# Optimization experiments

Measured on AMD Instinct MI355X. Metric: run time of the kernel, lower is better.

Reference implementation:

```python
import jax, jax.numpy as jnp
import numpy as np

B, L, N, C = 64, 12, 4096, 3
FD, HD, OUT = 32, 64, 12
TID, DIW, TD = 288, 7, 16
STEPS = 4
EMB = 10  # node embedding dim for learned adjacency


def setup_inputs() -> dict:
    key = jax.random.key(0)
    ks = jax.random.split(key, 16)
    g = lambda i, shape, s=0.05: jax.random.normal(ks[i], shape, dtype=jnp.float32) * s
    z = lambda n: jnp.zeros((n,), jnp.float32)
    return {
        "history_data": jax.random.uniform(ks[0], (B, L, N, C), dtype=jnp.float32),
        "future_data": jnp.zeros((B, L, N, 1), jnp.float32),
        "batch_seen": 0,
        "epoch": 0,
        "train": 1,
        "tid_emb": g(1, (TID, TD)),
        "diw_emb": g(2, (DIW, TD)),
        "t2f_w": g(3, (2 * TD, FD)), "t2f_b": z(FD),
        "enc_w1": g(4, (L * C, HD)), "enc_b1": z(HD),
        "enc_w2": g(5, (HD, FD)), "enc_b2": z(FD),
        "node_emb": g(6, (N, EMB), 1.0),
        "pde_w1": g(7, (FD, HD)), "pde_b1": z(HD),
        "pde_w2": g(8, (HD, FD)), "pde_b2": z(FD),
        "ss_win": g(9, (FD, FD)), "ss_wst": g(10, (FD, FD)), "ss_b": z(FD),
        "ss_wout": g(11, (FD, FD)), "ss_bout": z(FD),
        "dec_w1": g(12, (FD, HD)), "dec_b1": z(HD),
        "dec_w2": g(13, (HD, OUT)), "dec_b2": z(OUT),
        "pde_mix": jnp.array(0.5, jnp.float32),
    }


def reference(history_data, future_data, batch_seen, epoch, train,
              tid_emb, diw_emb, t2f_w, t2f_b,
              enc_w1, enc_b1, enc_w2, enc_b2,
              node_emb,
              pde_w1, pde_b1, pde_w2, pde_b2,
              ss_win, ss_wst, ss_b, ss_wout, ss_bout,
              dec_w1, dec_b1, dec_w2, dec_b2, pde_mix):
    # --- encoder: per-node MLP over flattened (L, C) history ---
    x = history_data[..., :C]                                    # [B,L,N,C]
    x = jnp.transpose(x, (0, 2, 1, 3)).reshape(B, N, L * C)      # [B,N,L*C]
    field = jnp.maximum(x @ enc_w1 + enc_b1, 0.0) @ enc_w2 + enc_b2  # [B,N,FD]

    # --- temporal field bias from last-step tid/diw ---
    tid_idx = jnp.clip((history_data[:, -1, :, 1] * TID).astype(jnp.int32), 0, TID - 1)
    diw_idx = jnp.clip((history_data[:, -1, :, 2] * DIW).astype(jnp.int32), 0, DIW - 1)
    temp = jnp.concatenate([tid_emb[tid_idx], diw_emb[diw_idx]], axis=-1)  # [B,N,2*TD]
    field = field + temp @ t2f_w + t2f_b

    # --- learned adjacency for graph Laplacian (L = I - A) ---
    A = jax.nn.softmax(jnp.maximum(node_emb @ node_emb.T, 0.0), axis=-1)  # [N,N]

    alpha = jax.nn.sigmoid(pde_mix)
    dt = 1.0 / STEPS
    state = jnp.zeros_like(field)
    for _ in range(STEPS):  # fixed small unroll over PDE steps
        L_F = jnp.einsum('nm,bmf->bnf', A, field) - field         # (A - I) F
        N_F = jnp.maximum(field @ pde_w1 + pde_b1, 0.0) @ pde_w2 + pde_b2
        fe = field + (alpha * L_F + (1.0 - alpha) * N_F) * dt
        state = jnp.tanh(fe @ ss_win + state @ ss_wst + ss_b)     # state-space update
        field = fe + state @ ss_wout + ss_bout

    # --- decoder: per-node MLP to output horizon ---
    pred = jnp.maximum(field @ dec_w1 + dec_b1, 0.0) @ dec_w2 + dec_b2  # [B,N,OUT]
    return jnp.transpose(pred, (0, 2, 1))[..., None]              # [B,OUT,N,1]
```

## Files before the change

### kernel.cpp

```cpp
#include <hip/hip_runtime.h>

#define BATCH 64
#define LHIST 12
#define NNODE 4096
#define CCH   3
#define FD    32
#define HD    64
#define OUTD  12
#define TIDN  288
#define DIWN  7
#define TDD   16
#define EMBD  10
#define MROWS 2048
#define KDIM  4096
#define MTOT  (BATCH * NNODE)

typedef __attribute__((ext_vector_type(8))) short bf16x8;
typedef __attribute__((ext_vector_type(4))) float f32x4;

union BF8U { bf16x8 v; unsigned short s[8]; };

__device__ __forceinline__ unsigned short f2b(float f) {
    union { float f; unsigned u; } v; v.f = f;
    unsigned r = v.u + 0x7fffu + ((v.u >> 16) & 1u);
    return (unsigned short)(r >> 16);
}

__device__ __forceinline__ float b2f(unsigned short u) {
    union { unsigned u; float f; } v; v.u = (unsigned)u << 16; return v.f;
}

__device__ __forceinline__ float fast_tanh(float x) {
    x = fminf(fmaxf(x, -15.f), 15.f);
    const float e = __expf(2.f * x);
    return (e - 1.f) / (e + 1.f);
}

__device__ __forceinline__ bf16x8 ldsfrag(const unsigned short* p) {
    return *(const bf16x8*)p;
}

__device__ __forceinline__ bf16x8 pack8(float4 a, float4 b) {
    BF8U u;
    u.s[0] = f2b(a.x); u.s[1] = f2b(a.y); u.s[2] = f2b(a.z); u.s[3] = f2b(a.w);
    u.s[4] = f2b(b.x); u.s[5] = f2b(b.y); u.s[6] = f2b(b.z); u.s[7] = f2b(b.w);
    return u.v;
}

__global__ __launch_bounds__(256) void build_A(const float* __restrict__ emb,
                                               unsigned short* __restrict__ A) {
    const int n = blockIdx.x;
    const int tid = threadIdx.x;
    __shared__ float sc[NNODE];
    __shared__ float red[256];
    float e[EMBD];
#pragma unroll
    for (int c = 0; c < EMBD; c++) e[c] = emb[(size_t)n * EMBD + c];
    float mx = 0.f;
    for (int m = tid; m < NNODE; m += 256) {
        float s = 0.f;
#pragma unroll
        for (int c = 0; c < EMBD; c++) s += e[c] * emb[(size_t)m * EMBD + c];
        s = fmaxf(s, 0.f);
        sc[m] = s;
        mx = fmaxf(mx, s);
    }
    red[tid] = mx;
    __syncthreads();
    for (int off = 128; off > 0; off >>= 1) {
        if (tid < off) red[tid] = fmaxf(red[tid], red[tid + off]);
        __syncthreads();
    }
    mx = red[0];
    __syncthreads();
    float sum = 0.f;
    for (int m = tid; m < NNODE; m += 256) {
        float v = expf(sc[m] - mx);
        sc[m] = v;
        sum += v;
    }
    red[tid] = sum;
    __syncthreads();
    for (int off = 128; off > 0; off >>= 1) {
        if (tid < off) red[tid] += red[tid + off];
        __syncthreads();
    }
    const float inv = 1.f / red[0];
    for (int m = tid; m < NNODE; m += 256)
        A[(size_t)n * NNODE + m] = f2b(sc[m] * inv);
}

__global__ __launch_bounds__(256, 2) void encoder(const float* __restrict__ hist,
                                                  const float* __restrict__ tid_emb,
                                                  const float* __restrict__ diw_emb,
                                                  const float* __restrict__ t2f_w,
                                                  const float* __restrict__ t2f_b,
                                                  const float* __restrict__ enc_w1,
                                                  const float* __restrict__ enc_b1,
                                                  const float* __restrict__ enc_w2,
                                                  const float* __restrict__ enc_b2,
                                                  float* __restrict__ field,
                                                  unsigned short* __restrict__ fT) {
    const int gid = blockIdx.x * 256 + threadIdx.x;
    const int b = gid >> 12;
    const int n = gid & (NNODE - 1);
    const float* hb = hist + ((size_t)b * LHIST * NNODE + n) * CCH;
    float x[LHIST * CCH];
#pragma unroll
    for (int l = 0; l < LHIST; l++) {
        x[l * 3 + 0] = hb[(size_t)l * NNODE * CCH + 0];
        x[l * 3 + 1] = hb[(size_t)l * NNODE * CCH + 1];
        x[l * 3 + 2] = hb[(size_t)l * NNODE * CCH + 2];
    }
    float f[FD];
#pragma unroll
    for (int o = 0; o < FD; o++) f[o] = enc_b2[o] + t2f_b[o];
    for (int j = 0; j < HD; j++) {
        float h = enc_b1[j];
#pragma unroll
        for (int k = 0; k < LHIST * CCH; k++) h += x[k] * enc_w1[k * HD + j];
        h = fmaxf(h, 0.f);
#pragma unroll
        for (int o = 0; o < FD; o++) f[o] += h * enc_w2[j * FD + o];
    }
    const int ti = min(max((int)(x[11 * 3 + 1] * 288.0f), 0), TIDN - 1);
    const int di = min(max((int)(x[11 * 3 + 2] * 7.0f), 0), DIWN - 1);
    for (int g = 0; g < TDD; g++) {
        const float tg = tid_emb[ti * TDD + g];
        const float dg = diw_emb[di * TDD + g];
#pragma unroll
        for (int o = 0; o < FD; o++)
            f[o] += tg * t2f_w[g * FD + o] + dg * t2f_w[(TDD + g) * FD + o];
    }
#pragma unroll
    for (int o4 = 0; o4 < FD / 4; o4++) {
        float4 v = {f[o4 * 4 + 0], f[o4 * 4 + 1], f[o4 * 4 + 2], f[o4 * 4 + 3]};
        *(float4*)&field[(size_t)gid * FD + o4 * 4] = v;
    }
#pragma unroll
    for (int o = 0; o < FD; o++)
        fT[(size_t)(b * FD + o) * NNODE + n] = f2b(f[o]);
}

__global__ __launch_bounds__(256) void gemm_bt(const unsigned short* __restrict__ X,
                                               const unsigned short* __restrict__ Y,
                                               unsigned short* __restrict__ Cp) {
    constexpr int K = KDIM;
    constexpr int KS = KDIM / 2;
    constexpr int BK = 32;
    __shared__ __align__(16) unsigned short Xs[2][128 * BK];
    __shared__ __align__(16) unsigned short Ys[2][128 * BK];
    const int tid = threadIdx.x;
    const int wave = tid >> 6;
    const int lane = tid & 63;

    const int l = blockIdx.x + 16 * blockIdx.y;
    const int xcd = l & 7;
    const int rem = l >> 3;
    const int by = xcd * 4 + (rem & 3);
    const int bx = rem >> 2;
    const int i0 = bx * 128;
    const int j0 = by * 128;
    const int k0 = blockIdx.z * KS;
    unsigned short* C = Cp + (size_t)blockIdx.z * MTOT * FD;

    const int wi = (wave >> 1) * 64;
    const int wj = (wave & 1) * 64;

    const int lrow = lane >> 2;
    const int gcol = (lane & 3) * 8;
    const int scol = ((lane & 3) ^ ((lane >> 3) & 3)) * 8;

    const unsigned short* Xg = X + (size_t)(i0 + wave * 32 + lrow) * K + k0 + gcol;
    const unsigned short* Yg = Y + (size_t)(j0 + wave * 32 + lrow) * K + k0 + gcol;
    const int ldoff0 = (wave * 32 + lrow) * BK + scol;
    const int ldoff1 = (wave * 32 + 16 + lrow) * BK + scol;

    const f32x4 zero = {0.f, 0.f, 0.f, 0.f};
    f32x4 acc[4][4];
#pragma unroll
    for (int a = 0; a < 4; a++)
#pragma unroll
        for (int b = 0; b < 4; b++) acc[a][b] = zero;

    const int fr = lane & 15;
    const int q = lane >> 4;
    const int kq = (q ^ ((fr >> 1) & 3)) * 8;

    uint4 rx0 = *(const uint4*)(Xg);
    uint4 rx1 = *(const uint4*)(Xg + 16 * K);
    uint4 ry0 = *(const uint4*)(Yg);
    uint4 ry1 = *(const uint4*)(Yg + 16 * K);
    *(uint4*)&Xs[0][ldoff0] = rx0;
    *(uint4*)&Xs[0][ldoff1] = rx1;
    *(uint4*)&Ys[0][ldoff0] = ry0;
    *(uint4*)&Ys[0][ldoff1] = ry1;
    __syncthreads();

    int p = 0;
    for (int kt = 0; kt < KS; kt += BK) {
        const bool more = (kt + BK < KS);
        if (more) {
            rx0 = *(const uint4*)(Xg + kt + BK);
            rx1 = *(const uint4*)(Xg + kt + BK + 16 * K);
            ry0 = *(const uint4*)(Yg + kt + BK);
            ry1 = *(const uint4*)(Yg + kt + BK + 16 * K);
        }
        bf16x8 fa[4], fb[4];
#pragma unroll
        for (int t = 0; t < 4; t++)
            fa[t] = *(const bf16x8*)&Xs[p][(wi + t * 16 + fr) * BK + kq];
#pragma unroll
        for (int t = 0; t < 4; t++)
            fb[t] = *(const bf16x8*)&Ys[p][(wj + t * 16 + fr) * BK + kq];
#pragma unroll
        for (int mi = 0; mi < 4; mi++)
#pragma unroll
            for (int ni = 0; ni < 4; ni++)
                acc[mi][ni] = __builtin_amdgcn_mfma_f32_16x16x32_bf16(
                    fa[mi], fb[ni], acc[mi][ni], 0, 0, 0);
        if (more) {
            const int np = p ^ 1;
            *(uint4*)&Xs[np][ldoff0] = rx0;
            *(uint4*)&Xs[np][ldoff1] = rx1;
            *(uint4*)&Ys[np][ldoff0] = ry0;
            *(uint4*)&Ys[np][ldoff1] = ry1;
            __syncthreads();
            p = np;
        }
    }

    const int r0 = q * 4;
#pragma unroll
    for (int mi = 0; mi < 4; mi++) {
#pragma unroll
        for (int ni = 0; ni < 4; ni++) {
            const int R0 = i0 + wi + mi * 16 + r0;
            const int col = j0 + wj + ni * 16 + fr;
            const size_t addr = ((size_t)(R0 >> 5) * NNODE + col) * FD + (R0 & 31);
            ushort4 pk = {f2b(acc[mi][ni][0]), f2b(acc[mi][ni][1]),
                          f2b(acc[mi][ni][2]), f2b(acc[mi][ni][3])};
            *(ushort4*)&C[addr] = pk;
        }
    }
}

#define HPAD 72
#define FPAD 40
__global__ __launch_bounds__(256, 2) void step_mfma(const unsigned short* __restrict__ Ct0,
                                                    const unsigned short* __restrict__ Ct1,
                                                    float* __restrict__ field,
                                                    unsigned short* __restrict__ state,
                                                    unsigned short* __restrict__ fT,
                                                    const float* __restrict__ pde_w1,
                                                    const float* __restrict__ pde_b1,
                                                    const float* __restrict__ pde_w2,
                                                    const float* __restrict__ pde_b2,
                                                    const float* __restrict__ ss_win,
                                                    const float* __restrict__ ss_wst,
                                                    const float* __restrict__ ss_b,
                                                    const float* __restrict__ ss_wout,
                                                    const float* __restrict__ ss_bout,
                                                    const float* __restrict__ pde_mix,
                                                    const float* __restrict__ dec_w1,
                                                    const float* __restrict__ dec_b1,
                                                    const float* __restrict__ dec_w2,
                                                    const float* __restrict__ dec_b2,
                                                    float* __restrict__ out,
                                                    int first, int last) {
    __shared__ __align__(16) unsigned short W1T[HD * FD];
    __shared__ __align__(16) unsigned short W2T[FD * HD];
    __shared__ __align__(16) unsigned short WinT[FD * FD];
    __shared__ __align__(16) unsigned short WstT[FD * FD];
    __shared__ __align__(16) unsigned short WoutT[FD * FD];
    __shared__ __align__(16) unsigned short Wd1T[HD * FD];
    __shared__ __align__(16) unsigned short Wd2T[16 * HD];
    __shared__ __align__(16) unsigned short Hs[4 * 64 * HPAD];
    __shared__ __align__(16) unsigned short Fs[4 * 64 * FPAD];

    const int tid = threadIdx.x;
    for (int i = tid; i < HD * FD; i += 256) W1T[(i & 63) * FD + (i >> 6)] = f2b(pde_w1[i]);
    for (int i = tid; i < HD * FD; i += 256) W2T[(i & 31) * HD + (i >> 5)] = f2b(pde_w2[i]);
    for (int i = tid; i < FD * FD; i += 256) {
        WinT [(i & 31) * FD + (i >> 5)] = f2b(ss_win[i]);
        WstT [(i & 31) * FD + (i >> 5)] = f2b(ss_wst[i]);
        WoutT[(i & 31) * FD + (i >> 5)] = f2b(ss_wout[i]);
    }
    if (last) {
        for (int i = tid; i < HD * FD; i += 256)
            Wd1T[(i & 63) * FD + (i >> 6)] = f2b(dec_w1[i]);
        for (int i = tid; i < 16 * HD; i += 256) {
            const int o = i >> 6, j = i & 63;
            Wd2T[i] = (o < OUTD) ? f2b(dec_w2[j * OUTD + o]) : (unsigned short)0;
        }
    }
    __syncthreads();

    const int wv = tid >> 6;
    const int lane = tid & 63;
    const int ln = lane & 15;
    const int q = lane >> 4;
    const int kq = q * 8;
    const int r0 = q * 4;
    const int mw = blockIdx.x * 256 + wv * 64;
    const int b = mw >> 12;
    const int n0 = mw & (NNODE - 1);
    unsigned short* Hw = &Hs[wv * 64 * HPAD];
    unsigned short* Fw = &Fs[wv * 64 * FPAD];

    const float alpha = 1.f / (1.f + __expf(-pde_mix[0]));
    const float dt = 0.25f;

    bf16x8 w1f[4], w2f[2][2], winf[2], wstf[2], woutf[2];
#pragma unroll
    for (int nj = 0; nj < 4; nj++) w1f[nj] = ldsfrag(&W1T[(nj * 16 + ln) * FD + kq]);
#pragma unroll
    for (int nf = 0; nf < 2; nf++) {
#pragma unroll
        for (int kk = 0; kk < 2; kk++)
            w2f[nf][kk] = ldsfrag(&W2T[(nf * 16 + ln) * HD + kk * 32 + kq]);
        winf[nf]  = ldsfrag(&WinT [(nf * 16 + ln) * FD + kq]);
        wstf[nf]  = ldsfrag(&WstT [(nf * 16 + ln) * FD + kq]);
        woutf[nf] = ldsfrag(&WoutT[(nf * 16 + ln) * FD + kq]);
    }

    float b1v[4], b2v[2], bsv[2], bov[2];
#pragma unroll
    for (int nj = 0; nj < 4; nj++) b1v[nj] = pde_b1[nj * 16 + ln];
#pragma unroll
    for (int nf = 0; nf < 2; nf++) {
        b2v[nf] = pde_b2[nf * 16 + ln];
        bsv[nf] = ss_b[nf * 16 + ln];
        bov[nf] = ss_bout[nf * 16 + ln];
    }

    bf16x8 fA[4], stA[4];
#pragma unroll
    for (int mi = 0; mi < 4; mi++) {
        const float4* fp = (const float4*)&field[(size_t)(mw + mi * 16 + ln) * FD + kq];
        fA[mi] = pack8(fp[0], fp[1]);
    }
    if (!first) {
#pragma unroll
        for (int mi = 0; mi < 4; mi++)
            stA[mi] = *(const bf16x8*)&state[(size_t)(mw + mi * 16 + ln) * FD + kq];
    }

    const f32x4 zero = {0.f, 0.f, 0.f, 0.f};

    f32x4 hc[4][4];
#pragma unroll
    for (int mi = 0; mi < 4; mi++)
#pragma unroll
        for (int nj = 0; nj < 4; nj++)
            hc[mi][nj] = __builtin_amdgcn_mfma_f32_16x16x32_bf16(fA[mi], w1f[nj], zero, 0, 0, 0);
#pragma unroll
    for (int mi = 0; mi < 4; mi++)
#pragma unroll
        for (int nj = 0; nj < 4; nj++)
#pragma unroll
            for (int r = 0; r < 4; r++)
                Hw[(mi * 16 + r0 + r) * HPAD + nj * 16 + ln] =
                    f2b(fmaxf(hc[mi][nj][r] + b1v[nj], 0.f));

    float fld[4][2][4], ctv[4][2][4];
#pragma unroll
    for (int mi = 0; mi < 4; mi++)
#pragma unroll
        for (int nf = 0; nf < 2; nf++)
#pragma unroll
            for (int r = 0; r < 4; r++) {
                const size_t idx = (size_t)(mw + mi * 16 + r0 + r) * FD + nf * 16 + ln;
                fld[mi][nf][r] = field[idx];
                ctv[mi][nf][r] = b2f(Ct0[idx]) + b2f(Ct1[idx]);
            }

    bf16x8 hA[4][2];
#pragma unroll
    for (int mi = 0; mi < 4; mi++)
#pragma unroll
        for (int kk = 0; kk < 2; kk++)
            hA[mi][kk] = ldsfrag(&Hw[(mi * 16 + ln) * HPAD + kk * 32 + kq]);
    f32x4 nc[4][2];
#pragma unroll
    for (int mi = 0; mi < 4; mi++)
#pragma unroll
        for (int nf = 0; nf < 2; nf++) {
            f32x4 a = __builtin_amdgcn_mfma_f32_16x16x32_bf16(hA[mi][0], w2f[nf][0], zero, 0, 0, 0);
            nc[mi][nf] = __builtin_amdgcn_mfma_f32_16x16x32_bf16(hA[mi][1], w2f[nf][1], a, 0, 0, 0);
        }

    float fe[4][2][4];
#pragma unroll
    for (int mi = 0; mi < 4; mi++)
#pragma unroll
        for (int nf = 0; nf < 2; nf++)
#pragma unroll
            for (int r = 0; r < 4; r++) {
                const float nfv = nc[mi][nf][r] + b2v[nf];
                const float fv = fld[mi][nf][r];
                fe[mi][nf][r] = fv + (alpha * (ctv[mi][nf][r] - fv) + (1.f - alpha) * nfv) * dt;
                Fw[(mi * 16 + r0 + r) * FPAD + nf * 16 + ln] = f2b(fe[mi][nf][r]);
            }

    bf16x8 feA[4];
#pragma unroll
    for (int mi = 0; mi < 4; mi++) feA[mi] = ldsfrag(&Fw[(mi * 16 + ln) * FPAD + kq]);
    f32x4 sc_[4][2];
#pragma unroll
    for (int mi = 0; mi < 4; mi++)
#pragma unroll
        for (int nf = 0; nf < 2; nf++) {
            f32x4 a = __builtin_amdgcn_mfma_f32_16x16x32_bf16(feA[mi], winf[nf], zero, 0, 0, 0);
            if (!first)
                a = __builtin_amdgcn_mfma_f32_16x16x32_bf16(stA[mi], wstf[nf], a, 0, 0, 0);
            sc_[mi][nf] = a;
        }
    float sval[4][2][4];
#pragma unroll
    for (int mi = 0; mi < 4; mi++)
#pragma unroll
        for (int nf = 0; nf < 2; nf++)
#pragma unroll
            for (int r = 0; r < 4; r++)
                sval[mi][nf][r] = fast_tanh(sc_[mi][nf][r] + bsv[nf]);
#pragma unroll
    for (int mi = 0; mi < 4; mi++)
#pragma unroll
        for (int nf = 0; nf < 2; nf++)
#pragma unroll
            for (int r = 0; r < 4; r++)
                Fw[(mi * 16 + r0 + r) * FPAD + nf * 16 + ln] = f2b(sval[mi][nf][r]);

    bf16x8 SA[4];
#pragma unroll
    for (int mi = 0; mi < 4; mi++) SA[mi] = ldsfrag(&Fw[(mi * 16 + ln) * FPAD + kq]);
    float fnew[4][2][4];
#pragma unroll
    for (int mi = 0; mi < 4; mi++)
#pragma unroll
        for (int nf = 0; nf < 2; nf++) {
            f32x4 oc = __builtin_amdgcn_mfma_f32_16x16x32_bf16(SA[mi], woutf[nf], zero, 0, 0, 0);
#pragma unroll
            for (int r = 0; r < 4; r++)
                fnew[mi][nf][r] = fe[mi][nf][r] + oc[r] + bov[nf];
        }

    if (!last) {
#pragma unroll
        for (int mi = 0; mi < 4; mi++) {
#pragma unroll
            for (int nf = 0; nf < 2; nf++) {
#pragma unroll
                for (int r = 0; r < 4; r++) {
                    const size_t idx = (size_t)(mw + mi * 16 + r0 + r) * FD + nf * 16 + ln;
                    field[idx] = fnew[mi][nf][r];
                    state[idx] = f2b(sval[mi][nf][r]);
                }
                ushort4 pk = {f2b(fnew[mi][nf][0]), f2b(fnew[mi][nf][1]),
                              f2b(fnew[mi][nf][2]), f2b(fnew[mi][nf][3])};
                const size_t ft_addr = (size_t)(b * FD + nf * 16 + ln) * NNODE + n0 + mi * 16 + r0;
                *(ushort4*)&fT[ft_addr] = pk;
            }
        }
    } else {
        bf16x8 wd1f[4], wd2f[2];
#pragma unroll
        for (int nj = 0; nj < 4; nj++) wd1f[nj] = ldsfrag(&Wd1T[(nj * 16 + ln) * FD + kq]);
#pragma unroll
        for (int kk = 0; kk < 2; kk++) wd2f[kk] = ldsfrag(&Wd2T[ln * HD + kk * 32 + kq]);
        float db1v[4];
#pragma unroll
        for (int nj = 0; nj < 4; nj++) db1v[nj] = dec_b1[nj * 16 + ln];
        const float db2v = (ln < OUTD) ? dec_b2[ln] : 0.f;

#pragma unroll
        for (int mi = 0; mi < 4; mi++)
#pragma unroll
            for (int nf = 0; nf < 2; nf++)
#pragma unroll
                for (int r = 0; r < 4; r++)
                    Fw[(mi * 16 + r0 + r) * FPAD + nf * 16 + ln] = f2b(fnew[mi][nf][r]);
        bf16x8 fnA[4];
#pragma unroll
        for (int mi = 0; mi < 4; mi++) fnA[mi] = ldsfrag(&Fw[(mi * 16 + ln) * FPAD + kq]);

        f32x4 h2[4][4];
#pragma unroll
        for (int mi = 0; mi < 4; mi++)
#pragma unroll
            for (int nj = 0; nj < 4; nj++)
                h2[mi][nj] = __builtin_amdgcn_mfma_f32_16x16x32_bf16(fnA[mi], wd1f[nj], zero, 0, 0, 0);
#pragma unroll
        for (int mi = 0; mi < 4; mi++)
#pragma unroll
            for (int nj = 0; nj < 4; nj++)
#pragma unroll
                for (int r = 0; r < 4; r++)
                    Hw[(mi * 16 + r0 + r) * HPAD + nj * 16 + ln] =
                        f2b(fmaxf(h2[mi][nj][r] + db1v[nj], 0.f));
        bf16x8 h2A[4][2];
#pragma unroll
        for (int mi = 0; mi < 4; mi++)
#pragma unroll
            for (int kk = 0; kk < 2; kk++)
                h2A[mi][kk] = ldsfrag(&Hw[(mi * 16 + ln) * HPAD + kk * 32 + kq]);
#pragma unroll
        for (int mi = 0; mi < 4; mi++) {
            f32x4 a = __builtin_amdgcn_mfma_f32_16x16x32_bf16(h2A[mi][0], wd2f[0], zero, 0, 0, 0);
            a = __builtin_amdgcn_mfma_f32_16x16x32_bf16(h2A[mi][1], wd2f[1], a, 0, 0, 0);
            if (ln < OUTD) {
                float4 v = {a[0] + db2v, a[1] + db2v, a[2] + db2v, a[3] + db2v};
                *(float4*)&out[(size_t)(b * OUTD + ln) * NNODE + n0 + mi * 16 + r0] = v;
            }
        }
    }
}

extern "C" void kernel_launch(void* const* d_in, const int* in_sizes, int n_in,
                              void* d_out, int out_size, void* d_ws, size_t ws_size,
                              hipStream_t stream) {
    (void)in_sizes; (void)n_in; (void)out_size; (void)ws_size;
    const float* hist    = (const float*)d_in[0];
    const float* tid_emb = (const float*)d_in[5];
    const float* diw_emb = (const float*)d_in[6];
    const float* t2f_w   = (const float*)d_in[7];
    const float* t2f_b   = (const float*)d_in[8];
    const float* enc_w1  = (const float*)d_in[9];
    const float* enc_b1  = (const float*)d_in[10];
    const float* enc_w2  = (const float*)d_in[11];
    const float* enc_b2  = (const float*)d_in[12];
    const float* node_emb= (const float*)d_in[13];
    const float* pde_w1  = (const float*)d_in[14];
    const float* pde_b1  = (const float*)d_in[15];
    const float* pde_w2  = (const float*)d_in[16];
    const float* pde_b2  = (const float*)d_in[17];
    const float* ss_win  = (const float*)d_in[18];
    const float* ss_wst  = (const float*)d_in[19];
    const float* ss_b    = (const float*)d_in[20];
    const float* ss_wout = (const float*)d_in[21];
    const float* ss_bout = (const float*)d_in[22];
    const float* dec_w1  = (const float*)d_in[23];
    const float* dec_b1  = (const float*)d_in[24];
    const float* dec_w2  = (const float*)d_in[25];
    const float* dec_b2  = (const float*)d_in[26];
    const float* pde_mix = (const float*)d_in[27];

    char* w = (char*)d_ws;
    unsigned short* A_bf = (unsigned short*)w;  w += (size_t)KDIM * KDIM * 2;
    unsigned short* fT   = (unsigned short*)w;  w += (size_t)MROWS * KDIM * 2;
    float* field = (float*)w;                   w += (size_t)MTOT * FD * 4;
    unsigned short* state = (unsigned short*)w; w += (size_t)MTOT * FD * 2;
    unsigned short* Cp    = (unsigned short*)w; w += (size_t)2 * MTOT * FD * 2;

    build_A<<<NNODE, 256, 0, stream>>>(node_emb, A_bf);
    encoder<<<(BATCH * NNODE) / 256, 256, 0, stream>>>(hist, tid_emb, diw_emb, t2f_w,
                                                       t2f_b, enc_w1, enc_b1, enc_w2,
                                                       enc_b2, field, fT);
    for (int s = 0; s < 4; s++) {
        gemm_bt<<<dim3(16, 32, 2), 256, 0, stream>>>(fT, A_bf, Cp);
        step_mfma<<<MTOT / 256, 256, 0, stream>>>(
            Cp, Cp + (size_t)MTOT * FD, field, state, fT, pde_w1, pde_b1, pde_w2,
            pde_b2, ss_win, ss_wst, ss_b, ss_wout, ss_bout, pde_mix,
            dec_w1, dec_b1, dec_w2, dec_b2, (float*)d_out,
            s == 0 ? 1 : 0, s == 3 ? 1 : 0);
    }
}
```

Baseline: 732.0 us.

## Fuse adjacency GEMM with PDE step epilogue and merge init kernels

Fuses the A·F GEMM and the per-node PDE/state-space step into one kernel. Each GEMM tile runs its own epilogue from LDS-transposed accumulators, which removes the split-K partial buffer and its round-trip through global memory. Tile loads now go through global_load_lds direct-to-LDS copies, and the fT buffer is ping-ponged so the next step's input can be written while other blocks still read the old one. The adjacency build and the encoder are merged into one launch. In exchange, split-K is dropped, leaving 512 blocks each running the full K loop, and LDS use per block goes up.

```diff
diff --git a/kernel.cpp b/kernel.cpp
--- a/kernel.cpp
+++ b/kernel.cpp
@@ -36,6 +36,11 @@
     return (e - 1.f) / (e + 1.f);
 }
 
+__device__ __forceinline__ void gl2lds16(const void* g, void* l) {
+    __builtin_amdgcn_global_load_lds((__attribute__((address_space(1))) void*)(void*)g,
+                                     (__attribute__((address_space(3))) void*)l, 16, 0, 0);
+}
+
 __device__ __forceinline__ bf16x8 ldsfrag(const unsigned short* p) {
     return *(const bf16x8*)p;
 }
@@ -47,112 +52,156 @@
     return u.v;
 }
 
-__global__ __launch_bounds__(256) void build_A(const float* __restrict__ emb,
-                                               unsigned short* __restrict__ A) {
-    const int n = blockIdx.x;
-    const int tid = threadIdx.x;
+__global__ __launch_bounds__(256, 2) void init_k(const float* __restrict__ emb,
+                                                 unsigned short* __restrict__ A,
+                                                 const float* __restrict__ hist,
+                                                 const float* __restrict__ tid_emb,
+                                                 const float* __restrict__ diw_emb,
+                                                 const float* __restrict__ t2f_w,
+                                                 const float* __restrict__ t2f_b,
+                                                 const float* __restrict__ enc_w1,
+                                                 const float* __restrict__ enc_b1,
+                                                 const float* __restrict__ enc_w2,
+                                                 const float* __restrict__ enc_b2,
+                                                 float* __restrict__ field,
+                                                 unsigned short* __restrict__ fT) {
     __shared__ float sc[NNODE];
     __shared__ float red[256];
-    float e[EMBD];
-#pragma unroll
-    for (int c = 0; c < EMBD; c++) e[c] = emb[(size_t)n * EMBD + c];
-    float mx = 0.f;
-    for (int m = tid; m < NNODE; m += 256) {
-        float s = 0.f;
-#pragma unroll
-        for (int c = 0; c < EMBD; c++) s += e[c] * emb[(size_t)m * EMBD + c];
-        s = fmaxf(s, 0.f);
-        sc[m] = s;
-        mx = fmaxf(mx, s);
-    }
-    red[tid] = mx;
-    __syncthreads();
-    for (int off = 128; off > 0; off >>= 1) {
-        if (tid < off) red[tid] = fmaxf(red[tid], red[tid + off]);
+    const int tid = threadIdx.x;
+    if (blockIdx.x < NNODE) {
+        const int n = blockIdx.x;
+        float e[EMBD];
+#pragma unroll
+        for (int c = 0; c < EMBD; c++) e[c] = emb[(size_t)n * EMBD + c];
+        float mx = 0.f;
+        for (int m = tid; m < NNODE; m += 256) {
+            float s = 0.f;
+#pragma unroll
+            for (int c = 0; c < EMBD; c++) s += e[c] * emb[(size_t)m * EMBD + c];
+            s = fmaxf(s, 0.f);
+            sc[m] = s;
+            mx = fmaxf(mx, s);
+        }
+        red[tid] = mx;
         __syncthreads();
-    }
-    mx = red[0];
-    __syncthreads();
-    float sum = 0.f;
-    for (int m = tid; m < NNODE; m += 256) {
-        float v = expf(sc[m] - mx);
-        sc[m] = v;
-        sum += v;
-    }
-    red[tid] = sum;
-    __syncthreads();
-    for (int off = 128; off > 0; off >>= 1) {
-        if (tid < off) red[tid] += red[tid + off];
+        for (int off = 128; off > 0; off >>= 1) {
+            if (tid < off) red[tid] = fmaxf(red[tid], red[tid + off]);
+            __syncthreads();
+        }
+        mx = red[0];
         __syncthreads();
-    }
-    const float inv = 1.f / red[0];
-    for (int m = tid; m < NNODE; m += 256)
-        A[(size_t)n * NNODE + m] = f2b(sc[m] * inv);
-}
-
-__global__ __launch_bounds__(256, 2) void encoder(const float* __restrict__ hist,
-                                                  const float* __restrict__ tid_emb,
-                                                  const float* __restrict__ diw_emb,
-                                                  const float* __restrict__ t2f_w,
-                                                  const float* __restrict__ t2f_b,
-                                                  const float* __restrict__ enc_w1,
-                                                  const float* __restrict__ enc_b1,
-                                                  const float* __restrict__ enc_w2,
-                                                  const float* __restrict__ enc_b2,
-                                                  float* __restrict__ field,
-                                                  unsigned short* __restrict__ fT) {
-    const int gid = blockIdx.x * 256 + threadIdx.x;
-    const int b = gid >> 12;
-    const int n = gid & (NNODE - 1);
-    const float* hb = hist + ((size_t)b * LHIST * NNODE + n) * CCH;
-    float x[LHIST * CCH];
-#pragma unroll
-    for (int l = 0; l < LHIST; l++) {
-        x[l * 3 + 0] = hb[(size_t)l * NNODE * CCH + 0];
-        x[l * 3 + 1] = hb[(size_t)l * NNODE * CCH + 1];
-        x[l * 3 + 2] = hb[(size_t)l * NNODE * CCH + 2];
-    }
-    float f[FD];
-#pragma unroll
-    for (int o = 0; o < FD; o++) f[o] = enc_b2[o] + t2f_b[o];
-    for (int j = 0; j < HD; j++) {
-        float h = enc_b1[j];
-#pragma unroll
-        for (int k = 0; k < LHIST * CCH; k++) h += x[k] * enc_w1[k * HD + j];
-        h = fmaxf(h, 0.f);
-#pragma unroll
-        for (int o = 0; o < FD; o++) f[o] += h * enc_w2[j * FD + o];
-    }
-    const int ti = min(max((int)(x[11 * 3 + 1] * 288.0f), 0), TIDN - 1);
-    const int di = min(max((int)(x[11 * 3 + 2] * 7.0f), 0), DIWN - 1);
-    for (int g = 0; g < TDD; g++) {
-        const float tg = tid_emb[ti * TDD + g];
-        const float dg = diw_emb[di * TDD + g];
+        float sum = 0.f;
+        for (int m = tid; m < NNODE; m += 256) {
+            float v = expf(sc[m] - mx);
+            sc[m] = v;
+            sum += v;
+        }
+        red[tid] = sum;
+        __syncthreads();
+        for (int off = 128; off > 0; off >>= 1) {
+            if (tid < off) red[tid] += red[tid + off];
+            __syncthreads();
+        }
+        const float inv = 1.f / red[0];
+        for (int m = tid; m < NNODE; m += 256)
+            A[(size_t)n * NNODE + m] = f2b(sc[m] * inv);
+    } else {
+        const int gid = (blockIdx.x - NNODE) * 256 + tid;
+        const int b = gid >> 12;
+        const int n = gid & (NNODE - 1);
+        const float* hb = hist + ((size_t)b * LHIST * NNODE + n) * CCH;
+        float x[LHIST * CCH];
+#pragma unroll
+        for (int l = 0; l < LHIST; l++) {
+            x[l * 3 + 0] = hb[(size_t)l * NNODE * CCH + 0];
+            x[l * 3 + 1] = hb[(size_t)l * NNODE * CCH + 1];
+            x[l * 3 + 2] = hb[(size_t)l * NNODE * CCH + 2];
+        }
+        float f[FD];
+#pragma unroll
+        for (int o = 0; o < FD; o++) f[o] = enc_b2[o] + t2f_b[o];
+        for (int j = 0; j < HD; j++) {
+            float h = enc_b1[j];
+#pragma unroll
+            for (int k = 0; k < LHIST * CCH; k++) h += x[k] * enc_w1[k * HD + j];
+            h = fmaxf(h, 0.f);
+#pragma unroll
+            for (int o = 0; o < FD; o++) f[o] += h * enc_w2[j * FD + o];
+        }
+        const int ti = min(max((int)(x[11 * 3 + 1] * 288.0f), 0), TIDN - 1);
+        const int di = min(max((int)(x[11 * 3 + 2] * 7.0f), 0), DIWN - 1);
+        for (int g = 0; g < TDD; g++) {
+            const float tg = tid_emb[ti * TDD + g];
+            const float dg = diw_emb[di * TDD + g];
+#pragma unroll
+            for (int o = 0; o < FD; o++)
+                f[o] += tg * t2f_w[g * FD + o] + dg * t2f_w[(TDD + g) * FD + o];
+        }
+#pragma unroll
+        for (int o4 = 0; o4 < FD / 4; o4++) {
+            float4 v = {f[o4 * 4 + 0], f[o4 * 4 + 1], f[o4 * 4 + 2], f[o4 * 4 + 3]};
+            *(float4*)&field[(size_t)gid * FD + o4 * 4] = v;
+        }
 #pragma unroll
         for (int o = 0; o < FD; o++)
-            f[o] += tg * t2f_w[g * FD + o] + dg * t2f_w[(TDD + g) * FD + o];
-    }
-#pragma unroll
-    for (int o4 = 0; o4 < FD / 4; o4++) {
-        float4 v = {f[o4 * 4 + 0], f[o4 * 4 + 1], f[o4 * 4 + 2], f[o4 * 4 + 3]};
-        *(float4*)&field[(size_t)gid * FD + o4 * 4] = v;
-    }
-#pragma unroll
-    for (int o = 0; o < FD; o++)
-        fT[(size_t)(b * FD + o) * NNODE + n] = f2b(f[o]);
-}
-
-__global__ __launch_bounds__(256) void gemm_bt(const unsigned short* __restrict__ X,
-                                               const unsigned short* __restrict__ Y,
-                                               unsigned short* __restrict__ Cp) {
+            fT[(size_t)(b * FD + o) * NNODE + n] = f2b(f[o]);
+    }
+}
+
+#define TPAD 36
+#define QHP  72
+#define QFP  40
+__global__ __launch_bounds__(256) void gemm_step(const unsigned short* __restrict__ X,
+                                                 const unsigned short* __restrict__ Y,
+                                                 float* __restrict__ field,
+                                                 unsigned short* __restrict__ state,
+                                                 unsigned short* __restrict__ fTo,
+                                                 const float* __restrict__ pde_w1,
+                                                 const float* __restrict__ pde_b1,
+                                                 const float* __restrict__ pde_w2,
+                                                 const float* __restrict__ pde_b2,
+                                                 const float* __restrict__ ss_win,
+                                                 const float* __restrict__ ss_wst,
+                                                 const float* __restrict__ ss_b,
+                                                 const float* __restrict__ ss_wout,
+                                                 const float* __restrict__ ss_bout,
+                                                 const float* __restrict__ pde_mix,
+                                                 const float* __restrict__ dec_w1,
+                                                 const float* __restrict__ dec_b1,
+                                                 const float* __restrict__ dec_w2,
+                                                 const float* __restrict__ dec_b2,
+                                                 float* __restrict__ out,
+                                                 int first, int last) {
     constexpr int K = KDIM;
-    constexpr int KS = KDIM / 2;
     constexpr int BK = 32;
-    __shared__ __align__(16) unsigned short Xs[2][128 * BK];
-    __shared__ __align__(16) unsigned short Ys[2][128 * BK];
+    __shared__ __align__(16) unsigned short SM0[512 * TPAD];
+    __shared__ __align__(16) unsigned short W1T[HD * FD];
+    __shared__ __align__(16) unsigned short W2T[FD * HD];
+    __shared__ __align__(16) unsigned short WinT[FD * FD];
+    __shared__ __align__(16) unsigned short WstT[FD * FD];
+    __shared__ __align__(16) unsigned short WoutT[FD * FD];
+    __shared__ __align__(16) unsigned short Hs[4 * 32 * QHP];
+    __shared__ __align__(16) unsigned short Fs[4 * 32 * QFP];
+
     const int tid = threadIdx.x;
     const int wave = tid >> 6;
     const int lane = tid & 63;
+
+    for (int i = tid; i < HD * FD; i += 256) W1T[(i & 63) * FD + (i >> 6)] = f2b(pde_w1[i]);
+    for (int i = tid; i < HD * FD; i += 256) W2T[(i & 31) * HD + (i >> 5)] = f2b(pde_w2[i]);
+    for (int i = tid; i < FD * FD; i += 256) {
+        WinT [(i & 31) * FD + (i >> 5)] = f2b(ss_win[i]);
+        WstT [(i & 31) * FD + (i >> 5)] = f2b(ss_wst[i]);
+        WoutT[(i & 31) * FD + (i >> 5)] = f2b(ss_wout[i]);
+    }
+    if (last) {
+        for (int i = tid; i < HD * FD; i += 256)
+            Hs[(i & 63) * FD + (i >> 6)] = f2b(dec_w1[i]);
+        for (int i = tid; i < 16 * HD; i += 256) {
+            const int o = i >> 6, j = i & 63;
+            Hs[HD * FD + i] = (o < OUTD) ? f2b(dec_w2[j * OUTD + o]) : (unsigned short)0;
+        }
+    }
 
     const int l = blockIdx.x + 16 * blockIdx.y;
     const int xcd = l & 7;
@@ -161,20 +210,22 @@
     const int bx = rem >> 2;
     const int i0 = bx * 128;
     const int j0 = by * 128;
-    const int k0 = blockIdx.z * KS;
-    unsigned short* C = Cp + (size_t)blockIdx.z * MTOT * FD;
+    const int b0 = i0 >> 5;
 
     const int wi = (wave >> 1) * 64;
     const int wj = (wave & 1) * 64;
 
     const int lrow = lane >> 2;
-    const int gcol = (lane & 3) * 8;
-    const int scol = ((lane & 3) ^ ((lane >> 3) & 3)) * 8;
-
-    const unsigned short* Xg = X + (size_t)(i0 + wave * 32 + lrow) * K + k0 + gcol;
-    const unsigned short* Yg = Y + (size_t)(j0 + wave * 32 + lrow) * K + k0 + gcol;
-    const int ldoff0 = (wave * 32 + lrow) * BK + scol;
-    const int ldoff1 = (wave * 32 + 16 + lrow) * BK + scol;
+    const int gcol = ((lane & 3) ^ ((lane >> 3) & 3)) * 8;
+
+    const unsigned short* Xg = X + (size_t)(i0 + wave * 32 + lrow) * K + gcol;
+    const unsigned short* Yg = Y + (size_t)(j0 + wave * 32 + lrow) * K + gcol;
+    unsigned short* XsB = SM0;
+    unsigned short* YsB = SM0 + 8192;
+    unsigned short* Xd0 = XsB + (wave * 32) * BK;
+    unsigned short* Xd1 = XsB + (wave * 32 + 16) * BK;
+    unsigned short* Yd0 = YsB + (wave * 32) * BK;
+    unsigned short* Yd1 = YsB + (wave * 32 + 16) * BK;
 
     const f32x4 zero = {0.f, 0.f, 0.f, 0.f};
     f32x4 acc[4][4];
@@ -185,129 +236,58 @@
 
     const int fr = lane & 15;
     const int q = lane >> 4;
-    const int kq = (q ^ ((fr >> 1) & 3)) * 8;
-
-    uint4 rx0 = *(const uint4*)(Xg);
-    uint4 rx1 = *(const uint4*)(Xg + 16 * K);
-    uint4 ry0 = *(const uint4*)(Yg);
-    uint4 ry1 = *(const uint4*)(Yg + 16 * K);
-    *(uint4*)&Xs[0][ldoff0] = rx0;
-    *(uint4*)&Xs[0][ldoff1] = rx1;
-    *(uint4*)&Ys[0][ldoff0] = ry0;
-    *(uint4*)&Ys[0][ldoff1] = ry1;
+    const int kq8 = (q ^ ((fr >> 1) & 3)) * 8;
+
+#define GS_ISSUE(P, KT)                                        \
+    gl2lds16(Xg + (KT), Xd0 + (P) * 4096);                     \
+    gl2lds16(Xg + (KT) + 16 * K, Xd1 + (P) * 4096);            \
+    gl2lds16(Yg + (KT), Yd0 + (P) * 4096);                     \
+    gl2lds16(Yg + (KT) + 16 * K, Yd1 + (P) * 4096);
+
+#define GS_COMPUTE(P)                                                                 \
+    {                                                                                 \
+        bf16x8 fa[4], fb[4];                                                          \
+        _Pragma("unroll") for (int t = 0; t < 4; t++)                                 \
+            fa[t] = *(const bf16x8*)&XsB[(P) * 4096 + (wi + t * 16 + fr) * BK + kq8]; \
+        _Pragma("unroll") for (int t = 0; t < 4; t++)                                 \
+            fb[t] = *(const bf16x8*)&YsB[(P) * 4096 + (wj + t * 16 + fr) * BK + kq8]; \
+        _Pragma("unroll") for (int mi = 0; mi < 4; mi++)                              \
+            _Pragma("unroll") for (int ni = 0; ni < 4; ni++)                          \
+                acc[mi][ni] = __builtin_amdgcn_mfma_f32_16x16x32_bf16(                \
+                    fa[mi], fb[ni], acc[mi][ni], 0, 0, 0);                            \
+    }
+
+    GS_ISSUE(0, 0);
     __syncthreads();
-
     int p = 0;
-    for (int kt = 0; kt < KS; kt += BK) {
-        const bool more = (kt + BK < KS);
-        if (more) {
-            rx0 = *(const uint4*)(Xg + kt + BK);
-            rx1 = *(const uint4*)(Xg + kt + BK + 16 * K);
-            ry0 = *(const uint4*)(Yg + kt + BK);
-            ry1 = *(const uint4*)(Yg + kt + BK + 16 * K);
-        }
-        bf16x8 fa[4], fb[4];
-#pragma unroll
-        for (int t = 0; t < 4; t++)
-            fa[t] = *(const bf16x8*)&Xs[p][(wi + t * 16 + fr) * BK + kq];
-#pragma unroll
-        for (int t = 0; t < 4; t++)
-            fb[t] = *(const bf16x8*)&Ys[p][(wj + t * 16 + fr) * BK + kq];
-#pragma unroll
-        for (int mi = 0; mi < 4; mi++)
-#pragma unroll
-            for (int ni = 0; ni < 4; ni++)
-                acc[mi][ni] = __builtin_amdgcn_mfma_f32_16x16x32_bf16(
-                    fa[mi], fb[ni], acc[mi][ni], 0, 0, 0);
-        if (more) {
-            const int np = p ^ 1;
-            *(uint4*)&Xs[np][ldoff0] = rx0;
-            *(uint4*)&Xs[np][ldoff1] = rx1;
-            *(uint4*)&Ys[np][ldoff0] = ry0;
-            *(uint4*)&Ys[np][ldoff1] = ry1;
-            __syncthreads();
-            p = np;
-        }
-    }
-
+    for (int kt = 0; kt < K; kt += BK) {
+        if (kt + BK < K) { GS_ISSUE(p ^ 1, kt + BK); }
+        GS_COMPUTE(p);
+        __syncthreads();
+        p ^= 1;
+    }
+#undef GS_COMPUTE
+#undef GS_ISSUE
+
+    unsigned short* T = SM0;
     const int r0 = q * 4;
 #pragma unroll
     for (int mi = 0; mi < 4; mi++) {
 #pragma unroll
         for (int ni = 0; ni < 4; ni++) {
             const int R0 = i0 + wi + mi * 16 + r0;
-            const int col = j0 + wj + ni * 16 + fr;
-            const size_t addr = ((size_t)(R0 >> 5) * NNODE + col) * FD + (R0 & 31);
+            const int nl = wj + ni * 16 + fr;
             ushort4 pk = {f2b(acc[mi][ni][0]), f2b(acc[mi][ni][1]),
                           f2b(acc[mi][ni][2]), f2b(acc[mi][ni][3])};
-            *(ushort4*)&C[addr] = pk;
-        }
-    }
-}
-
-#define HPAD 72
-#define FPAD 40
-__global__ __launch_bounds__(256, 2) void step_mfma(const unsigned short* __restrict__ Ct0,
-                                                    const unsigned short* __restrict__ Ct1,
-                                                    float* __restrict__ field,
-                                                    unsigned short* __restrict__ state,
-                                                    unsigned short* __restrict__ fT,
-                                                    const float* __restrict__ pde_w1,
-                                                    const float* __restrict__ pde_b1,
-                                                    const float* __restrict__ pde_w2,
-                                                    const float* __restrict__ pde_b2,
-                                                    const float* __restrict__ ss_win,
-                                                    const float* __restrict__ ss_wst,
-                                                    const float* __restrict__ ss_b,
-                                                    const float* __restrict__ ss_wout,
-                                                    const float* __restrict__ ss_bout,
-                                                    const float* __restrict__ pde_mix,
-                                                    const float* __restrict__ dec_w1,
-                                                    const float* __restrict__ dec_b1,
-                                                    const float* __restrict__ dec_w2,
-                                                    const float* __restrict__ dec_b2,
-                                                    float* __restrict__ out,
-                                                    int first, int last) {
-    __shared__ __align__(16) unsigned short W1T[HD * FD];
-    __shared__ __align__(16) unsigned short W2T[FD * HD];
-    __shared__ __align__(16) unsigned short WinT[FD * FD];
-    __shared__ __align__(16) unsigned short WstT[FD * FD];
-    __shared__ __align__(16) unsigned short WoutT[FD * FD];
-    __shared__ __align__(16) unsigned short Wd1T[HD * FD];
-    __shared__ __align__(16) unsigned short Wd2T[16 * HD];
-    __shared__ __align__(16) unsigned short Hs[4 * 64 * HPAD];
-    __shared__ __align__(16) unsigned short Fs[4 * 64 * FPAD];
-
-    const int tid = threadIdx.x;
-    for (int i = tid; i < HD * FD; i += 256) W1T[(i & 63) * FD + (i >> 6)] = f2b(pde_w1[i]);
-    for (int i = tid; i < HD * FD; i += 256) W2T[(i & 31) * HD + (i >> 5)] = f2b(pde_w2[i]);
-    for (int i = tid; i < FD * FD; i += 256) {
-        WinT [(i & 31) * FD + (i >> 5)] = f2b(ss_win[i]);
-        WstT [(i & 31) * FD + (i >> 5)] = f2b(ss_wst[i]);
-        WoutT[(i & 31) * FD + (i >> 5)] = f2b(ss_wout[i]);
-    }
-    if (last) {
-        for (int i = tid; i < HD * FD; i += 256)
-            Wd1T[(i & 63) * FD + (i >> 6)] = f2b(dec_w1[i]);
-        for (int i = tid; i < 16 * HD; i += 256) {
-            const int o = i >> 6, j = i & 63;
-            Wd2T[i] = (o < OUTD) ? f2b(dec_w2[j * OUTD + o]) : (unsigned short)0;
+            *(ushort4*)&T[((((R0 >> 5) & 3) << 7) + nl) * TPAD + (R0 & 31)] = pk;
         }
     }
     __syncthreads();
 
-    const int wv = tid >> 6;
-    const int lane = tid & 63;
-    const int ln = lane & 15;
-    const int q = lane >> 4;
+    const int ln = fr;
     const int kq = q * 8;
-    const int r0 = q * 4;
-    const int mw = blockIdx.x * 256 + wv * 64;
-    const int b = mw >> 12;
-    const int n0 = mw & (NNODE - 1);
-    unsigned short* Hw = &Hs[wv * 64 * HPAD];
-    unsigned short* Fw = &Fs[wv * 64 * FPAD];
-
+    unsigned short* Hw = &Hs[wave * 32 * QHP];
+    unsigned short* Fw = &Fs[wave * 32 * QFP];
     const float alpha = 1.f / (1.f + __expf(-pde_mix[0]));
     const float dt = 0.25f;
 
@@ -323,7 +303,6 @@
         wstf[nf]  = ldsfrag(&WstT [(nf * 16 + ln) * FD + kq]);
         woutf[nf] = ldsfrag(&WoutT[(nf * 16 + ln) * FD + kq]);
     }
-
     float b1v[4], b2v[2], bsv[2], bov[2];
 #pragma unroll
     for (int nj = 0; nj < 4; nj++) b1v[nj] = pde_b1[nj * 16 + ln];
@@ -334,184 +313,194 @@
         bov[nf] = ss_bout[nf * 16 + ln];
     }
 
-    bf16x8 fA[4], stA[4];
-#pragma unroll
-    for (int mi = 0; mi < 4; mi++) {
-        const float4* fp = (const float4*)&field[(size_t)(mw + mi * 16 + ln) * FD + kq];
-        fA[mi] = pack8(fp[0], fp[1]);
-    }
-    if (!first) {
-#pragma unroll
-        for (int mi = 0; mi < 4; mi++)
-            stA[mi] = *(const bf16x8*)&state[(size_t)(mw + mi * 16 + ln) * FD + kq];
-    }
-
-    const f32x4 zero = {0.f, 0.f, 0.f, 0.f};
-
-    f32x4 hc[4][4];
-#pragma unroll
-    for (int mi = 0; mi < 4; mi++)
-#pragma unroll
-        for (int nj = 0; nj < 4; nj++)
-            hc[mi][nj] = __builtin_amdgcn_mfma_f32_16x16x32_bf16(fA[mi], w1f[nj], zero, 0, 0, 0);
-#pragma unroll
-    for (int mi = 0; mi < 4; mi++)
-#pragma unroll
-        for (int nj = 0; nj < 4; nj++)
-#pragma unroll
-            for (int r = 0; r < 4; r++)
-                Hw[(mi * 16 + r0 + r) * HPAD + nj * 16 + ln] =
-                    f2b(fmaxf(hc[mi][nj][r] + b1v[nj], 0.f));
-
-    float fld[4][2][4], ctv[4][2][4];
-#pragma unroll
-    for (int mi = 0; mi < 4; mi++)
-#pragma unroll
-        for (int nf = 0; nf < 2; nf++)
-#pragma unroll
-            for (int r = 0; r < 4; r++) {
-                const size_t idx = (size_t)(mw + mi * 16 + r0 + r) * FD + nf * 16 + ln;
-                fld[mi][nf][r] = field[idx];
-                ctv[mi][nf][r] = b2f(Ct0[idx]) + b2f(Ct1[idx]);
+    bf16x8 wd1f[4], wd2f[2];
+    float db1v[4];
+    float db2v = 0.f;
+    if (last) {
+#pragma unroll
+        for (int nj = 0; nj < 4; nj++) wd1f[nj] = ldsfrag(&Hs[(nj * 16 + ln) * FD + kq]);
+#pragma unroll
+        for (int kk = 0; kk < 2; kk++) wd2f[kk] = ldsfrag(&Hs[HD * FD + ln * HD + kk * 32 + kq]);
+#pragma unroll
+        for (int nj = 0; nj < 4; nj++) db1v[nj] = dec_b1[nj * 16 + ln];
+        db2v = (ln < OUTD) ? dec_b2[ln] : 0.f;
+        __syncthreads();
+    }
+
+    for (int qtr = 0; qtr < 4; qtr++) {
+        const int lb = wave * 128 + qtr * 32;
+        const int bb = lb >> 7;
+        const int nl0 = lb & 127;
+        const int bg = b0 + bb;
+        const int mwg = (bg << 12) + j0 + nl0;
+
+        bf16x8 fA[2], stA[2];
+#pragma unroll
+        for (int mi = 0; mi < 2; mi++) {
+            const float4* fp = (const float4*)&field[(size_t)(mwg + mi * 16 + ln) * FD + kq];
+            fA[mi] = pack8(fp[0], fp[1]);
+        }
+        if (!first) {
+#pragma unroll
+            for (int mi = 0; mi < 2; mi++)
+                stA[mi] = *(const bf16x8*)&state[(size_t)(mwg + mi * 16 + ln) * FD + kq];
+        }
+
+        f32x4 hc[2][4];
+#pragma unroll
+        for (int mi = 0; mi < 2; mi++)
+#pragma unroll
+            for (int nj = 0; nj < 4; nj++)
+                hc[mi][nj] = __builtin_amdgcn_mfma_f32_16x16x32_bf16(fA[mi], w1f[nj], zero, 0, 0, 0);
+#pragma unroll
+        for (int mi = 0; mi < 2; mi++)
+#pragma unroll
+            for (int nj = 0; nj < 4; nj++)
+#pragma unroll
+                for (int r = 0; r < 4; r++)
+                    Hw[(mi * 16 + r0 + r) * QHP + nj * 16 + ln] =
+                        f2b(fmaxf(hc[mi][nj][r] + b1v[nj], 0.f));
+
+        float fld[2][2][4], ctv[2][2][4];
+#pragma unroll
+        for (int mi = 0; mi < 2; mi++)
+#pragma unroll
+            for (int nf = 0; nf < 2; nf++)
+#pragma unroll
+                for (int r = 0; r < 4; r++) {
+                    const size_t idx = (size_t)(mwg + mi * 16 + r0 + r) * FD + nf * 16 + ln;
+                    fld[mi][nf][r] = field[idx];
+                    ctv[mi][nf][r] = b2f(T[(lb + mi * 16 + r0 + r) * TPAD + nf * 16 + ln]);
+                }
+
+        bf16x8 hA[2][2];
+#pragma unroll
+        for (int mi = 0; mi < 2; mi++)
+#pragma unroll
+            for (int kk = 0; kk < 2; kk++)
+                hA[mi][kk] = ldsfrag(&Hw[(mi * 16 + ln) * QHP + kk * 32 + kq]);
+        f32x4 nc[2][2];
+#pragma unroll
+        for (int mi = 0; mi < 2; mi++)
+#pragma unroll
+            for (int nf = 0; nf < 2; nf++) {
+                f32x4 a = __builtin_amdgcn_mfma_f32_16x16x32_bf16(hA[mi][0], w2f[nf][0], zero, 0, 0, 0);
+                nc[mi][nf] = __builtin_amdgcn_mfma_f32_16x16x32_bf16(hA[mi][1], w2f[nf][1], a, 0, 0, 0);
             }
 
-    bf16x8 hA[4][2];
-#pragma unroll
-    for (int mi = 0; mi < 4; mi++)
-#pragma unroll
-        for (int kk = 0; kk < 2; kk++)
-            hA[mi][kk] = ldsfrag(&Hw[(mi * 16 + ln) * HPAD + kk * 32 + kq]);
-    f32x4 nc[4][2];
-#pragma unroll
-    for (int mi = 0; mi < 4; mi++)
-#pragma unroll
-        for (int nf = 0; nf < 2; nf++) {
-            f32x4 a = __builtin_amdgcn_mfma_f32_16x16x32_bf16(hA[mi][0], w2f[nf][0], zero, 0, 0, 0);
-            nc[mi][nf] = __builtin_amdgcn_mfma_f32_16x16x32_bf16(hA[mi][1], w2f[nf][1], a, 0, 0, 0);
-        }
-
-    float fe[4][2][4];
-#pragma unroll
-    for (int mi = 0; mi < 4; mi++)
-#pragma unroll
-        for (int nf = 0; nf < 2; nf++)
-#pragma unroll
-            for (int r = 0; r < 4; r++) {
-                const float nfv = nc[mi][nf][r] + b2v[nf];
-                const float fv = fld[mi][nf][r];
-                fe[mi][nf][r] = fv + (alpha * (ctv[mi][nf][r] - fv) + (1.f - alpha) * nfv) * dt;
-                Fw[(mi * 16 + r0 + r) * FPAD + nf * 16 + ln] = f2b(fe[mi][nf][r]);
+        float fe[2][2][4];
+#pragma unroll
+        for (int mi = 0; mi < 2; mi++)
+#pragma unroll
+            for (int nf = 0; nf < 2; nf++)
+#pragma unroll
+                for (int r = 0; r < 4; r++) {
+                    const float nfv = nc[mi][nf][r] + b2v[nf];
+                    const float fv = fld[mi][nf][r];
+                    fe[mi][nf][r] = fv + (alpha * (ctv[mi][nf][r] - fv) + (1.f - alpha) * nfv) * dt;
+                    Fw[(mi * 16 + r0 + r) * QFP + nf * 16 + ln] = f2b(fe[mi][nf][r]);
+                }
+
+        bf16x8 feA[2];
+#pragma unroll
+        for (int mi = 0; mi < 2; mi++) feA[mi] = ldsfrag(&Fw[(mi * 16 + ln) * QFP + kq]);
+        f32x4 sc_[2][2];
+#pragma unroll
+        for (int mi = 0; mi < 2; mi++)
+#pragma unroll
+            for (int nf = 0; nf < 2; nf++) {
+                f32x4 a = __builtin_amdgcn_mfma_f32_16x16x32_bf16(feA[mi], winf[nf], zero, 0, 0, 0);
+                if (!first)
+                    a = __builtin_amdgcn_mfma_f32_16x16x32_bf16(stA[mi], wstf[nf], a, 0, 0, 0);
+                sc_[mi][nf] = a;
             }
-
-    bf16x8 feA[4];
-#pragma unroll
-    for (int mi = 0; mi < 4; mi++) feA[mi] = ldsfrag(&Fw[(mi * 16 + ln) * FPAD + kq]);
-    f32x4 sc_[4][2];
-#pragma unroll
-    for (int mi = 0; mi < 4; mi++)
-#pragma unroll
-        for (int nf = 0; nf < 2; nf++) {
-            f32x4 a = __builtin_amdgcn_mfma_f32_16x16x32_bf16(feA[mi], winf[nf], zero, 0, 0, 0);
-            if (!first)
-                a = __builtin_amdgcn_mfma_f32_16x16x32_bf16(stA[mi], wstf[nf], a, 0, 0, 0);
-            sc_[mi][nf] = a;
-        }
-    float sval[4][2][4];
-#pragma unroll
-    for (int mi = 0; mi < 4; mi++)
-#pragma unroll
-        for (int nf = 0; nf < 2; nf++)
-#pragma unroll
-            for (int r = 0; r < 4; r++)
-                sval[mi][nf][r] = fast_tanh(sc_[mi][nf][r] + bsv[nf]);
-#pragma unroll
-    for (int mi = 0; mi < 4; mi++)
-#pragma unroll
-        for (int nf = 0; nf < 2; nf++)
-#pragma unroll
-            for (int r = 0; r < 4; r++)
-                Fw[(mi * 16 + r0 + r) * FPAD + nf * 16 + ln] = f2b(sval[mi][nf][r]);
-
-    bf16x8 SA[4];
-#pragma unroll
-    for (int mi = 0; mi < 4; mi++) SA[mi] = ldsfrag(&Fw[(mi * 16 + ln) * FPAD + kq]);
-    float fnew[4][2][4];
-#pragma unroll
-    for (int mi = 0; mi < 4; mi++)
-#pragma unroll
-        for (int nf = 0; nf < 2; nf++) {
-            f32x4 oc = __builtin_amdgcn_mfma_f32_16x16x32_bf16(SA[mi], woutf[nf], zero, 0, 0, 0);
-#pragma unroll
-            for (int r = 0; r < 4; r++)
-                fnew[mi][nf][r] = fe[mi][nf][r] + oc[r] + bov[nf];
-        }
-
-    if (!last) {
-#pragma unroll
-        for (int mi = 0; mi < 4; mi++) {
+        float sval[2][2][4];
+#pragma unroll
+        for (int mi = 0; mi < 2; mi++)
+#pragma unroll
+            for (int nf = 0; nf < 2; nf++)
+#pragma unroll
+                for (int r = 0; r < 4; r++)
+                    sval[mi][nf][r] = fast_tanh(sc_[mi][nf][r] + bsv[nf]);
+#pragma unroll
+        for (int mi = 0; mi < 2; mi++)
+#pragma unroll
+            for (int nf = 0; nf < 2; nf++)
+#pragma unroll
+                for (int r = 0; r < 4; r++)
+                    Fw[(mi * 16 + r0 + r) * QFP + nf * 16 + ln] = f2b(sval[mi][nf][r]);
+
+        bf16x8 SA[2];
+#pragma unroll
+        for (int mi = 0; mi < 2; mi++) SA[mi] = ldsfrag(&Fw[(mi * 16 + ln) * QFP + kq]);
+        float fnew[2][2][4];
+#pragma unroll
+        for (int mi = 0; mi < 2; mi++)
 #pragma unroll
             for (int nf = 0; nf < 2; nf++) {
-#pragma unroll
-                for (int r = 0; r < 4; r++) {
-                    const size_t idx = (size_t)(mw + mi * 16 + r0 + r) * FD + nf * 16 + ln;
-                    field[idx] = fnew[mi][nf][r];
-                    state[idx] = f2b(sval[mi][nf][r]);
+                f32x4 oc = __builtin_amdgcn_mfma_f32_16x16x32_bf16(SA[mi], woutf[nf], zero, 0, 0, 0);
+#pragma unroll
+                for (int r = 0; r < 4; r++)
+                    fnew[mi][nf][r] = fe[mi][nf][r] + oc[r] + bov[nf];
+            }
+
+        if (!last) {
+#pragma unroll
+            for (int mi = 0; mi < 2; mi++) {
+#pragma unroll
+                for (int nf = 0; nf < 2; nf++) {
+#pragma unroll
+                    for (int r = 0; r < 4; r++) {
+                        const size_t idx = (size_t)(mwg + mi * 16 + r0 + r) * FD + nf * 16 + ln;
+                        field[idx] = fnew[mi][nf][r];
+                        state[idx] = f2b(sval[mi][nf][r]);
+                    }
+                    ushort4 pk = {f2b(fnew[mi][nf][0]), f2b(fnew[mi][nf][1]),
+                                  f2b(fnew[mi][nf][2]), f2b(fnew[mi][nf][3])};
+                    const size_t fta = (size_t)(bg * FD + nf * 16 + ln) * NNODE
+                                     + j0 + nl0 + mi * 16 + r0;
+                    *(ushort4*)&fTo[fta] = pk;
                 }
-                ushort4 pk = {f2b(fnew[mi][nf][0]), f2b(fnew[mi][nf][1]),
-                              f2b(fnew[mi][nf][2]), f2b(fnew[mi][nf][3])};
-                const size_t ft_addr = (size_t)(b * FD + nf * 16 + ln) * NNODE + n0 + mi * 16 + r0;
-                *(ushort4*)&fT[ft_addr] = pk;
             }
-        }
-    } else {
-        bf16x8 wd1f[4], wd2f[2];
-#pragma unroll
-        for (int nj = 0; nj < 4; nj++) wd1f[nj] = ldsfrag(&Wd1T[(nj * 16 + ln) * FD + kq]);
-#pragma unroll
-        for (int kk = 0; kk < 2; kk++) wd2f[kk] = ldsfrag(&Wd2T[ln * HD + kk * 32 + kq]);
-        float db1v[4];
-#pragma unroll
-        for (int nj = 0; nj < 4; nj++) db1v[nj] = dec_b1[nj * 16 + ln];
-        const float db2v = (ln < OUTD) ? dec_b2[ln] : 0.f;
-
-#pragma unroll
-        for (int mi = 0; mi < 4; mi++)
-#pragma unroll
-            for (int nf = 0; nf < 2; nf++)
-#pragma unroll
-                for (int r = 0; r < 4; r++)
-                    Fw[(mi * 16 + r0 + r) * FPAD + nf * 16 + ln] = f2b(fnew[mi][nf][r]);
-        bf16x8 fnA[4];
-#pragma unroll
-        for (int mi = 0; mi < 4; mi++) fnA[mi] = ldsfrag(&Fw[(mi * 16 + ln) * FPAD + kq]);
-
-        f32x4 h2[4][4];
-#pragma unroll
-        for (int mi = 0; mi < 4; mi++)
-#pragma unroll
-            for (int nj = 0; nj < 4; nj++)
-                h2[mi][nj] = __builtin_amdgcn_mfma_f32_16x16x32_bf16(fnA[mi], wd1f[nj], zero, 0, 0, 0);
-#pragma unroll
-        for (int mi = 0; mi < 4; mi++)
-#pragma unroll
-            for (int nj = 0; nj < 4; nj++)
-#pragma unroll
-                for (int r = 0; r < 4; r++)
-                    Hw[(mi * 16 + r0 + r) * HPAD + nj * 16 + ln] =
-                        f2b(fmaxf(h2[mi][nj][r] + db1v[nj], 0.f));
-        bf16x8 h2A[4][2];
-#pragma unroll
-        for (int mi = 0; mi < 4; mi++)
-#pragma unroll
-            for (int kk = 0; kk < 2; kk++)
-                h2A[mi][kk] = ldsfrag(&Hw[(mi * 16 + ln) * HPAD + kk * 32 + kq]);
-#pragma unroll
-        for (int mi = 0; mi < 4; mi++) {
-            f32x4 a = __builtin_amdgcn_mfma_f32_16x16x32_bf16(h2A[mi][0], wd2f[0], zero, 0, 0, 0);
-            a = __builtin_amdgcn_mfma_f32_16x16x32_bf16(h2A[mi][1], wd2f[1], a, 0, 0, 0);
-            if (ln < OUTD) {
-                float4 v = {a[0] + db2v, a[1] + db2v, a[2] + db2v, a[3] + db2v};
-                *(float4*)&out[(size_t)(b * OUTD + ln) * NNODE + n0 + mi * 16 + r0] = v;
+        } else {
+#pragma unroll
+            for (int mi = 0; mi < 2; mi++)
+#pragma unroll
+                for (int nf = 0; nf < 2; nf++)
+#pragma unroll
+                    for (int r = 0; r < 4; r++)
+                        Fw[(mi * 16 + r0 + r) * QFP + nf * 16 + ln] = f2b(fnew[mi][nf][r]);
+            bf16x8 fnA[2];
+#pragma unroll
+            for (int mi = 0; mi < 2; mi++) fnA[mi] = ldsfrag(&Fw[(mi * 16 + ln) * QFP + kq]);
+            f32x4 h2[2][4];
+#pragma unroll
+            for (int mi = 0; mi < 2; mi++)
+#pragma unroll
+                for (int nj = 0; nj < 4; nj++)
+                    h2[mi][nj] = __builtin_amdgcn_mfma_f32_16x16x32_bf16(fnA[mi], wd1f[nj], zero, 0, 0, 0);
+#pragma unroll
+            for (int mi = 0; mi < 2; mi++)
+#pragma unroll
+                for (int nj = 0; nj < 4; nj++)
+#pragma unroll
+                    for (int r = 0; r < 4; r++)
+                        Hw[(mi * 16 + r0 + r) * QHP + nj * 16 + ln] =
+                            f2b(fmaxf(h2[mi][nj][r] + db1v[nj], 0.f));
+            bf16x8 h2A[2][2];
+#pragma unroll
+            for (int mi = 0; mi < 2; mi++)
+#pragma unroll
+                for (int kk = 0; kk < 2; kk++)
+                    h2A[mi][kk] = ldsfrag(&Hw[(mi * 16 + ln) * QHP + kk * 32 + kq]);
+#pragma unroll
+            for (int mi = 0; mi < 2; mi++) {
+                f32x4 a = __builtin_amdgcn_mfma_f32_16x16x32_bf16(h2A[mi][0], wd2f[0], zero, 0, 0, 0);
+                a = __builtin_amdgcn_mfma_f32_16x16x32_bf16(h2A[mi][1], wd2f[1], a, 0, 0, 0);
+                if (ln < OUTD) {
+                    float4 v = {a[0] + db2v, a[1] + db2v, a[2] + db2v, a[3] + db2v};
+                    *(float4*)&out[(size_t)(bg * OUTD + ln) * NNODE + j0 + nl0 + mi * 16 + r0] = v;
+                }
             }
         }
     }
@@ -548,20 +537,19 @@
 
     char* w = (char*)d_ws;
     unsigned short* A_bf = (unsigned short*)w;  w += (size_t)KDIM * KDIM * 2;
-    unsigned short* fT   = (unsigned short*)w;  w += (size_t)MROWS * KDIM * 2;
+    unsigned short* fTa  = (unsigned short*)w;  w += (size_t)MROWS * KDIM * 2;
+    unsigned short* fTb  = (unsigned short*)w;  w += (size_t)MROWS * KDIM * 2;
     float* field = (float*)w;                   w += (size_t)MTOT * FD * 4;
     unsigned short* state = (unsigned short*)w; w += (size_t)MTOT * FD * 2;
-    unsigned short* Cp    = (unsigned short*)w; w += (size_t)2 * MTOT * FD * 2;
-
-    build_A<<<NNODE, 256, 0, stream>>>(node_emb, A_bf);
-    encoder<<<(BATCH * NNODE) / 256, 256, 0, stream>>>(hist, tid_emb, diw_emb, t2f_w,
-                                                       t2f_b, enc_w1, enc_b1, enc_w2,
-                                                       enc_b2, field, fT);
+
+    init_k<<<NNODE + MTOT / 256, 256, 0, stream>>>(node_emb, A_bf, hist, tid_emb,
+                                                   diw_emb, t2f_w, t2f_b, enc_w1,
+                                                   enc_b1, enc_w2, enc_b2, field, fTa);
+    unsigned short* fts[5] = {fTa, fTb, fTa, fTb, fTa};
     for (int s = 0; s < 4; s++) {
-        gemm_bt<<<dim3(16, 32, 2), 256, 0, stream>>>(fT, A_bf, Cp);
-        step_mfma<<<MTOT / 256, 256, 0, stream>>>(
-            Cp, Cp + (size_t)MTOT * FD, field, state, fT, pde_w1, pde_b1, pde_w2,
-            pde_b2, ss_win, ss_wst, ss_b, ss_wout, ss_bout, pde_mix,
+        gemm_step<<<dim3(16, 32), 256, 0, stream>>>(
+            fts[s], A_bf, field, state, fts[s + 1], pde_w1, pde_b1, pde_w2, pde_b2,
+            ss_win, ss_wst, ss_b, ss_wout, ss_bout, pde_mix,
             dec_w1, dec_b1, dec_w2, dec_b2, (float*)d_out,
             s == 0 ? 1 : 0, s == 3 ? 1 : 0);
     }
```

Result: slower. 983.1 us (+34.3%).
